# Kernel optimization log

Hardware: AMD Instinct MI355X
Metric: run time of the kernel (lower is better)

Reference implementation:

```python
import jax, jax.numpy as jnp
import numpy as np

B, N, K = 8, 4096, 16
C_IN = 3
MLP = (64, 64, 128)


def _init_conv(key, c_out, c_in):
    kw, kb = jax.random.split(key)
    bound = 1.0 / np.sqrt(c_in)
    W = jax.random.uniform(kw, (c_out, c_in), jnp.float32, -bound, bound)
    b = jax.random.uniform(kb, (c_out,), jnp.float32, -bound, bound)
    return W, b


def setup_inputs() -> dict:
    key = jax.random.key(0)
    k0, k1, k2, k3 = jax.random.split(key, 4)
    xyz = jax.random.normal(k0, (B, C_IN, N), jnp.float32)
    W0, b0 = _init_conv(k1, MLP[0], C_IN)
    W1, b1 = _init_conv(k2, MLP[1], MLP[0])
    W2, b2 = _init_conv(k3, MLP[2], MLP[1])
    return {"xyz": xyz, "W0": W0, "b0": b0, "W1": W1, "b1": b1, "W2": W2, "b2": b2}


def reference(xyz, W0, b0, W1, b1, W2, b2):
    # xyz: [B, 3, N] -> pts: [B, N, 3]
    pts = jnp.transpose(xyz, (0, 2, 1))
    # KNN: squared pairwise distances [B, N, N]
    sq = jnp.sum(pts * pts, axis=-1)  # [B, N]
    d2 = sq[:, :, None] + sq[:, None, :] - 2.0 * jnp.einsum('bnc,bmc->bnm', pts, pts)
    _, idx = jax.lax.top_k(-d2, K)  # [B, N, K] indices of K nearest (incl. self)
    # gather neighbor coords: [B, N, K, 3]
    grouped = jax.vmap(lambda p, i: p[i])(pts, idx)
    # center-relative coordinates
    rel = grouped - pts[:, :, None, :]  # [B, N, K, 3]
    # three 1x1 conv (= per-point linear) + ReLU layers
    h = jax.nn.relu(jnp.einsum('bnkc,oc->bnko', rel, W0) + b0)
    h = jax.nn.relu(jnp.einsum('bnkc,oc->bnko', h, W1) + b1)
    h = jax.nn.relu(jnp.einsum('bnkc,oc->bnko', h, W2) + b2)
    # max over K neighbors -> [B, N, D'] -> [B, D', N]
    out = jnp.max(h, axis=2)
    return jnp.transpose(out, (0, 2, 1))
```

## Files before the change

### kernel.cpp

```cpp
#include <hip/hip_runtime.h>
#include <cstddef>

#define NB   8
#define NPTS 4096
#define KNN  16
#define FCAP 64

typedef _Float16 h2 __attribute__((ext_vector_type(2)));
typedef _Float16 h8 __attribute__((ext_vector_type(8)));
typedef float    f4 __attribute__((ext_vector_type(4)));
typedef float    f16f __attribute__((ext_vector_type(16)));

static __device__ __forceinline__ h2 pk2(float a, float b) {
    return __builtin_bit_cast(h2, __builtin_amdgcn_cvt_pkrtz(a, b));
}
static __device__ __forceinline__ unsigned bch(h2 v) {
    return __builtin_bit_cast(unsigned, v);
}

#if __has_builtin(__builtin_amdgcn_fmed3f)
static __device__ __forceinline__ float MED3(float a, float b, float c) {
    return __builtin_amdgcn_fmed3f(a, b, c);
}
#else
static __device__ __forceinline__ float MED3(float a, float b, float c) {
    return fmaxf(fminf(a, b), fminf(fmaxf(a, b), c));
}
#endif

static __device__ __forceinline__ float dist2(float4 Q, float4 p) {
    float dot = fmaf(Q.z, p.z, fmaf(Q.y, p.y, Q.x * p.x));
    return fmaf(-2.0f, dot, Q.w + p.w);
}

__global__ __launch_bounds__(256) void prep_kernel(const float* __restrict__ xyz,
                                                   float4* __restrict__ pts4) {
    int i = blockIdx.x * 256 + threadIdx.x;
    int b = i >> 12;
    int n = i & (NPTS - 1);
    const float* base = xyz + (size_t)b * 3 * NPTS;
    float x = base[n];
    float y = base[NPTS + n];
    float z = base[2 * NPTS + n];
    float sq = fmaf(z, z, fmaf(y, y, x * x));
    pts4[i] = make_float4(x, y, z, sq);
}

__global__ __launch_bounds__(1024, 8) void knn_kernel(const float4* __restrict__ pts4,
                                                      int* __restrict__ idxout) {
    __shared__ uint2 Pm[NPTS];
    __shared__ char  sbuf[16384];
    __shared__ float tauv[64];
    __shared__ int   qcnt[64];
    __shared__ unsigned pmaxu, smaxu;

    float*    partials = (float*)sbuf;
    unsigned* fidx     = (unsigned*)sbuf;
    float*    fdist    = (float*)Pm;

    int tid = threadIdx.x;
    int b   = blockIdx.y;
    const float4* pb = pts4 + (size_t)b * NPTS;

    if (tid == 0) { pmaxu = 0u; smaxu = 0u; }
    __syncthreads();

    {
        float lm = 0.0f, ls = 0.0f;
        for (int j = tid; j < NPTS; j += 1024) {
            float4 p = pb[j];
            lm = fmaxf(lm, fmaxf(fabsf(p.x), fmaxf(fabsf(p.y), fabsf(p.z))));
            ls = fmaxf(ls, p.w);
            h2 lo = { (_Float16)p.x, (_Float16)p.y };
            h2 hi = { (_Float16)p.z, (_Float16)p.w };
            Pm[j].x = bch(lo);
            Pm[j].y = bch(hi);
        }
        atomicMax(&pmaxu, __builtin_bit_cast(unsigned, lm));
        atomicMax(&smaxu, __builtin_bit_cast(unsigned, ls));
    }

    int wave = tid >> 6, lane = tid & 63;
    int g  = wave >> 3;
    int c  = wave & 7;
    int col = lane & 31;
    int hl  = lane >> 5;
    int q  = g * 32 + col;
    int nq = (blockIdx.x << 6) + q;
    int cbase = c * 512;

    float4 qf = pb[nq];
    float uxf = -2.0f * qf.x, uyf = -2.0f * qf.y, uzf = -2.0f * qf.z;
    _Float16 uxh = (_Float16)uxf, uyh = (_Float16)uyf, uzh = (_Float16)uzf;
    _Float16 uxl = (_Float16)(uxf - (float)uxh);
    _Float16 uyl = (_Float16)(uyf - (float)uyh);
    _Float16 uzl = (_Float16)(uzf - (float)uzh);
    uint4 bu = {0u, 0u, 0u, 0u};
    if (hl == 0) {
        h2 b01 = {uxh, uyh}, b23 = {uzh, (_Float16)1.0f};
        h2 b45 = {uxl, uyl}, b67 = {uzl, (_Float16)0.0f};
        bu.x = bch(b01); bu.y = bch(b23); bu.z = bch(b45); bu.w = bch(b67);
    }
    h8 bq = __builtin_bit_cast(h8, bu);
    __syncthreads();

    {
        float c0 = __builtin_inff(), c1 = c0, c2 = c0, c3 = c0;
#pragma unroll 2
        for (int t = 0; t < 16; ++t) {
            uint4 au = {0u, 0u, 0u, 0u};
            if (hl == 0) {
                uint2 pd = Pm[cbase + t * 32 + col];
                au.x = pd.x; au.y = pd.y; au.z = pd.x; au.w = pd.y;
            }
            f16f d = __builtin_amdgcn_mfma_f32_32x32x16_f16(
                __builtin_bit_cast(h8, au), bq, (f16f)0.0f, 0, 0, 0);
            float a0 = fminf(d[0], d[1]),   a1 = fminf(d[2], d[3]);
            float a2 = fminf(d[4], d[5]),   a3 = fminf(d[6], d[7]);
            float a4 = fminf(d[8], d[9]),   a5 = fminf(d[10], d[11]);
            float a6 = fminf(d[12], d[13]), a7 = fminf(d[14], d[15]);
            float b0 = fminf(a0, a1), b1 = fminf(a2, a3);
            float b2 = fminf(a4, a5), b3 = fminf(a6, a7);
            float rmin = fminf(fminf(b0, b1), fminf(b2, b3));
            float p0 = c0, p1 = c1, p2 = c2;
            c0 = fminf(p0, rmin);
            c1 = MED3(rmin, p0, c1);
            c2 = MED3(rmin, p1, c2);
            c3 = MED3(rmin, p2, c3);
        }
        int sb = (c * 2 + hl) * 4;
        partials[(sb + 0) * 64 + q] = c0;
        partials[(sb + 1) * 64 + q] = c1;
        partials[(sb + 2) * 64 + q] = c2;
        partials[(sb + 3) * 64 + q] = c3;
    }
    __syncthreads();

    if (tid < 256) {
        int qq = tid & 63, k = tid >> 6;
        float mb[16];
#pragma unroll
        for (int j = 0; j < 16; ++j) mb[j] = __builtin_inff();
        for (int s = 0; s < 16; ++s) {
            float v = partials[(k * 16 + s) * 64 + qq];
            float prev = mb[0];
            mb[0] = fminf(mb[0], v);
#pragma unroll
            for (int i = 1; i < 16; ++i) {
                float cur = mb[i];
                mb[i] = MED3(v, prev, cur);
                prev = cur;
            }
        }
#pragma unroll
        for (int j = 0; j < 16; ++j) partials[(k * 16 + j) * 64 + qq] = mb[j];
    }
    __syncthreads();

    if (tid < 64) {
        float mb[16];
#pragma unroll
        for (int j = 0; j < 16; ++j) mb[j] = __builtin_inff();
        for (int k = 0; k < 4; ++k) {
            for (int j = 0; j < 16; ++j) {
                float v = partials[(k * 16 + j) * 64 + tid];
                if (v >= mb[15]) break;
                float prev = mb[0];
                mb[0] = fminf(mb[0], v);
#pragma unroll
                for (int i = 1; i < 16; ++i) {
                    float cur = mb[i];
                    mb[i] = MED3(v, prev, cur);
                    prev = cur;
                }
            }
        }
        float4 q2 = pb[(blockIdx.x << 6) + tid];
        float sumq = fabsf(q2.x) + fabsf(q2.y) + fabsf(q2.z);
        float qn   = sqrtf(q2.w);
        float pmax = __builtin_bit_cast(float, pmaxu);
        float smax = __builtin_bit_cast(float, smaxu);
        const float r11c = 4.8828125e-4f;
        float tau = mb[15];
        float E0  = smax * r11c + 2.0f * sumq * pmax * r11c + 1.0e-3f;
        float rad2 = fmaxf(tau + 2.0f * E0 + q2.w, 0.0f);
        float R   = qn + sqrtf(rad2);
        float Eq  = (R * R + 2.0f * sumq * R) * r11c + 6.0e-4f;
        Eq = fminf(Eq, E0);
        tauv[tid] = tau + 2.0f * Eq;
        qcnt[tid] = 0;
    }
    __syncthreads();

    {
        float tc = tauv[q];
#pragma unroll 1
        for (int t = 0; t < 16; ++t) {
            uint4 au = {0u, 0u, 0u, 0u};
            if (hl == 0) {
                uint2 pd = Pm[cbase + t * 32 + col];
                au.x = pd.x; au.y = pd.y; au.z = pd.x; au.w = pd.y;
            }
            f16f d = __builtin_amdgcn_mfma_f32_32x32x16_f16(
                __builtin_bit_cast(h8, au), bq, (f16f)0.0f, 0, 0, 0);
            unsigned m = 0u;
#pragma unroll
            for (int r = 0; r < 16; ++r) m |= (d[r] <= tc) ? (1u << r) : 0u;
            if (m) {
                int pos = atomicAdd(&qcnt[q], __popc(m));
                while (m) {
                    int r = __ffs(m) - 1;
                    m &= m - 1;
                    if (pos < FCAP)
                        fidx[pos * 64 + q] =
                            (unsigned)(cbase + t * 32 + (r & 3) + 8 * (r >> 2) + 4 * hl);
                    ++pos;
                }
            }
        }
    }
    __syncthreads();

    for (int e = tid; e < FCAP * 64; e += 1024) {
        int j = e >> 6, qq = e & 63;
        int nc = qcnt[qq]; nc = nc > FCAP ? FCAP : nc;
        if (j < nc) {
            float4 Qf = pb[(blockIdx.x << 6) + qq];
            fdist[e] = dist2(Qf, pb[fidx[e]]);
        }
    }
    __syncthreads();

    if (tid < 64) {
        int nqf = (blockIdx.x << 6) + tid;
        float4 Qf = pb[nqf];
        float bd[16]; int bi[16];
#pragma unroll
        for (int j = 0; j < 16; ++j) { bd[j] = __builtin_inff(); bi[j] = 0; }
        int cnt = qcnt[tid];
        if (cnt <= FCAP) {
            for (int j = 0; j < cnt; ++j) {
                float x  = fdist[j * 64 + tid];
                int   xi = (int)fidx[j * 64 + tid];
                if (x < bd[15] || (x == bd[15] && xi < bi[15])) {
#pragma unroll
                    for (int t = 0; t < 16; ++t) {
                        bool cc = (x < bd[t]) || (x == bd[t] && xi < bi[t]);
                        float nd = cc ? x  : bd[t];
                        int   ni = cc ? xi : bi[t];
                        float od = cc ? bd[t] : x;
                        int   oi = cc ? bi[t] : xi;
                        bd[t] = nd; bi[t] = ni; x = od; xi = oi;
                    }
                }
            }
        } else {
            for (int m = 0; m < NPTS; ++m) {
                float x = dist2(Qf, pb[m]);
                int  xi = m;
                if (x < bd[15] || (x == bd[15] && xi < bi[15])) {
#pragma unroll
                    for (int t = 0; t < 16; ++t) {
                        bool cc = (x < bd[t]) || (x == bd[t] && xi < bi[t]);
                        float nd = cc ? x  : bd[t];
                        int   ni = cc ? xi : bi[t];
                        float od = cc ? bd[t] : x;
                        int   oi = cc ? bi[t] : xi;
                        bd[t] = nd; bi[t] = ni; x = od; xi = oi;
                    }
                }
            }
        }
        int* op = idxout + ((size_t)b * NPTS + nqf) * KNN;
#pragma unroll
        for (int j = 0; j < 16; ++j) op[j] = bi[j];
    }
}

__global__ __launch_bounds__(256, 2) void mlp_kernel(
    const float4* __restrict__ pts4, const int* __restrict__ idxin,
    const float* __restrict__ W0, const float* __restrict__ b0,
    const float* __restrict__ W1, const float* __restrict__ b1,
    const float* __restrict__ W2, const float* __restrict__ b2,
    float* __restrict__ out) {

    int tid  = threadIdx.x;
    int wave = tid >> 6, lane = tid & 63;
    int g = lane >> 4, i = lane & 15;

    h2 w0x[8], w0y[8], w0z[8], w0b[8];
#pragma unroll
    for (int s = 0; s < 2; ++s)
#pragma unroll
        for (int v = 0; v < 4; ++v) {
            int c0 = 32 * s + 8 * g + 2 * v;
            w0x[s * 4 + v] = pk2(W0[c0 * 3 + 0], W0[c0 * 3 + 3]);
            w0y[s * 4 + v] = pk2(W0[c0 * 3 + 1], W0[c0 * 3 + 4]);
            w0z[s * 4 + v] = pk2(W0[c0 * 3 + 2], W0[c0 * 3 + 5]);
            w0b[s * 4 + v] = pk2(b0[c0], b0[c0 + 1]);
        }
    h2 b1p[8];
#pragma unroll
    for (int s = 0; s < 2; ++s)
#pragma unroll
        for (int v = 0; v < 4; ++v) {
            int c0 = 32 * s + 16 * (v >> 1) + 4 * g + 2 * (v & 1);
            b1p[s * 4 + v] = pk2(b1[c0], b1[c0 + 1]);
        }
    h8 wf1[4][2];
#pragma unroll
    for (int t = 0; t < 4; ++t)
#pragma unroll
        for (int s = 0; s < 2; ++s) {
            const float* p = W1 + (16 * t + i) * 64 + 32 * s + 8 * g;
            h8 f;
#pragma unroll
            for (int j = 0; j < 8; ++j) f[j] = (_Float16)p[j];
            wf1[t][s] = f;
        }
    h8 wf2[8][2];
#pragma unroll
    for (int t = 0; t < 8; ++t)
#pragma unroll
        for (int s = 0; s < 2; ++s) {
            const float* p = W2 + (16 * t + i) * 64;
            h8 f;
#pragma unroll
            for (int j = 0; j < 8; ++j) {
                int vc = 32 * s + 16 * (j >> 2) + 4 * g + (j & 3);
                f[j] = (_Float16)p[vc];
            }
            wf2[t][s] = f;
        }

    int gw = blockIdx.x * 4 + wave;
    int b  = gw >> 8;
    int n0 = (gw & 255) * 16;

    const float4* pb = pts4 + (size_t)b * NPTS;
    float4 q = pb[n0 + i];
    const int* ip = idxin + ((size_t)b * NPTS + n0 + i) * KNN;

    float mx[8][4];
#pragma unroll
    for (int t = 0; t < 8; ++t)
#pragma unroll
        for (int r = 0; r < 4; ++r) mx[t][r] = -3.4e38f;

    for (int it = 0; it < KNN; ++it) {
        int mi = ip[it];
        float4 p = pb[mi];
        float rx = p.x - q.x, ry = p.y - q.y, rz = p.z - q.z;
        h2 rxx = pk2(rx, rx), ryy = pk2(ry, ry), rzz = pk2(rz, rz);

        h8 h0f[2];
#pragma unroll
        for (int s = 0; s < 2; ++s)
#pragma unroll
            for (int v = 0; v < 4; ++v) {
                h2 hh = __builtin_elementwise_fma(w0z[s * 4 + v], rzz,
                         __builtin_elementwise_fma(w0y[s * 4 + v], ryy,
                          __builtin_elementwise_fma(w0x[s * 4 + v], rxx, w0b[s * 4 + v])));
                hh = __builtin_elementwise_max(hh, (h2)(_Float16)0.0f);
                h0f[s][2 * v]     = hh.x;
                h0f[s][2 * v + 1] = hh.y;
            }

        f4 d1[4];
#pragma unroll
        for (int t = 0; t < 4; ++t) {
            d1[t] = (f4)0.0f;
#pragma unroll
            for (int s = 0; s < 2; ++s)
                d1[t] = __builtin_amdgcn_mfma_f32_16x16x32_f16(wf1[t][s], h0f[s], d1[t], 0, 0, 0);
        }

        h8 h1f[2];
#pragma unroll
        for (int s = 0; s < 2; ++s)
#pragma unroll
            for (int v = 0; v < 4; ++v) {
                int t = 2 * s + (v >> 1), r0 = 2 * (v & 1);
                h2 w = pk2(d1[t][r0], d1[t][r0 + 1]);
                w = w + b1p[s * 4 + v];
                w = __builtin_elementwise_max(w, (h2)(_Float16)0.0f);
                h1f[s][2 * v]     = w.x;
                h1f[s][2 * v + 1] = w.y;
            }

#pragma unroll
        for (int t = 0; t < 8; ++t) {
            f4 d2 = (f4)0.0f;
#pragma unroll
            for (int s = 0; s < 2; ++s)
                d2 = __builtin_amdgcn_mfma_f32_16x16x32_f16(wf2[t][s], h1f[s], d2, 0, 0, 0);
#pragma unroll
            for (int r = 0; r < 4; ++r) mx[t][r] = fmaxf(mx[t][r], d2[r]);
        }
    }

    size_t ob = (size_t)b * 128 * NPTS + n0 + i;
#pragma unroll
    for (int t = 0; t < 8; ++t)
#pragma unroll
        for (int r = 0; r < 4; ++r) {
            int chn = 16 * t + 4 * g + r;
            float v = fmaxf(mx[t][r] + b2[chn], 0.0f);
            out[ob + (size_t)chn * NPTS] = v;
        }
}

extern "C" void kernel_launch(void* const* d_in, const int* in_sizes, int n_in,
                              void* d_out, int out_size, void* d_ws, size_t ws_size,
                              hipStream_t stream) {
    (void)in_sizes; (void)n_in; (void)out_size; (void)ws_size;
    const float* xyz = (const float*)d_in[0];
    const float* W0  = (const float*)d_in[1];
    const float* b0  = (const float*)d_in[2];
    const float* W1  = (const float*)d_in[3];
    const float* b1  = (const float*)d_in[4];
    const float* W2  = (const float*)d_in[5];
    const float* b2  = (const float*)d_in[6];
    float* out = (float*)d_out;

    char* ws = (char*)d_ws;
    float4* pts4 = (float4*)ws;
    int*    idxb = (int*)(ws + (size_t)NB * NPTS * sizeof(float4));

    prep_kernel<<<dim3(NB * NPTS / 256), dim3(256), 0, stream>>>(xyz, pts4);
    knn_kernel<<<dim3(NPTS / 64, NB), dim3(1024), 0, stream>>>(pts4, idxb);
    mlp_kernel<<<dim3(512), dim3(256), 0, stream>>>(
        pts4, idxb, W0, b0, W1, b1, W2, b2, out);
}
```

Measured before the change: 107.6 us.

## Precompute fp16 point table and bounds in prep, shrink KNN blocks to 32 queries

The prep kernel now runs one block per batch. It writes the packed fp16 point table and the per-batch max bounds to global memory, using a wave-shuffle reduction. The KNN kernel stops rebuilding the 32 KB shared fp16 table in every block and reads the MFMA operands straight from global/L2. Blocks shrink to 512 threads with 32 queries each, so there are twice as many blocks and far less shared memory per block. The costs are a prep kernel with only 8 blocks, which serialises more work, and global-memory latency on the MFMA operand loads.

```diff
diff --git a/kernel.cpp b/kernel.cpp
--- a/kernel.cpp
+++ b/kernel.cpp
@@ -5,6 +5,7 @@
 #define NPTS 4096
 #define KNN  16
 #define FCAP 64
+#define QB   32
 
 typedef _Float16 h2 __attribute__((ext_vector_type(2)));
 typedef _Float16 h8 __attribute__((ext_vector_type(8)));
@@ -33,60 +34,66 @@
     return fmaf(-2.0f, dot, Q.w + p.w);
 }
 
-__global__ __launch_bounds__(256) void prep_kernel(const float* __restrict__ xyz,
-                                                   float4* __restrict__ pts4) {
-    int i = blockIdx.x * 256 + threadIdx.x;
-    int b = i >> 12;
-    int n = i & (NPTS - 1);
+__global__ __launch_bounds__(1024) void prep_kernel(const float* __restrict__ xyz,
+                                                    float4* __restrict__ pts4,
+                                                    uint2* __restrict__ pm16,
+                                                    unsigned* __restrict__ mx) {
+    __shared__ float wred[32];
+    int b = blockIdx.x, tid = threadIdx.x;
     const float* base = xyz + (size_t)b * 3 * NPTS;
-    float x = base[n];
-    float y = base[NPTS + n];
-    float z = base[2 * NPTS + n];
-    float sq = fmaf(z, z, fmaf(y, y, x * x));
-    pts4[i] = make_float4(x, y, z, sq);
-}
-
-__global__ __launch_bounds__(1024, 8) void knn_kernel(const float4* __restrict__ pts4,
-                                                      int* __restrict__ idxout) {
-    __shared__ uint2 Pm[NPTS];
-    __shared__ char  sbuf[16384];
-    __shared__ float tauv[64];
-    __shared__ int   qcnt[64];
-    __shared__ unsigned pmaxu, smaxu;
+    float lm = 0.0f, ls = 0.0f;
+    for (int j = tid; j < NPTS; j += 1024) {
+        float x = base[j];
+        float y = base[NPTS + j];
+        float z = base[2 * NPTS + j];
+        float sq = fmaf(z, z, fmaf(y, y, x * x));
+        pts4[(size_t)b * NPTS + j] = make_float4(x, y, z, sq);
+        h2 lo = { (_Float16)x, (_Float16)y };
+        h2 hi = { (_Float16)z, (_Float16)sq };
+        pm16[(size_t)b * NPTS + j] = make_uint2(bch(lo), bch(hi));
+        lm = fmaxf(lm, fmaxf(fabsf(x), fmaxf(fabsf(y), fabsf(z))));
+        ls = fmaxf(ls, sq);
+    }
+#pragma unroll
+    for (int o = 32; o; o >>= 1) {
+        lm = fmaxf(lm, __shfl_xor(lm, o));
+        ls = fmaxf(ls, __shfl_xor(ls, o));
+    }
+    int wave = tid >> 6, lane = tid & 63;
+    if (lane == 0) { wred[wave] = lm; wred[16 + wave] = ls; }
+    __syncthreads();
+    if (tid == 0) {
+        float m = wred[0], s = wred[16];
+#pragma unroll
+        for (int i = 1; i < 16; ++i) { m = fmaxf(m, wred[i]); s = fmaxf(s, wred[16 + i]); }
+        mx[b * 2 + 0] = __builtin_bit_cast(unsigned, m);
+        mx[b * 2 + 1] = __builtin_bit_cast(unsigned, s);
+    }
+}
+
+__global__ __launch_bounds__(512, 8) void knn_kernel(const float4* __restrict__ pts4,
+                                                     const uint2* __restrict__ pm16,
+                                                     const unsigned* __restrict__ mx,
+                                                     int* __restrict__ idxout) {
+    __shared__ char  sbuf[8192];
+    __shared__ float fdist[FCAP * QB];
+    __shared__ float tauv[QB];
+    __shared__ int   qcnt[QB];
 
     float*    partials = (float*)sbuf;
     unsigned* fidx     = (unsigned*)sbuf;
-    float*    fdist    = (float*)Pm;
 
     int tid = threadIdx.x;
     int b   = blockIdx.y;
-    const float4* pb = pts4 + (size_t)b * NPTS;
-
-    if (tid == 0) { pmaxu = 0u; smaxu = 0u; }
-    __syncthreads();
-
-    {
-        float lm = 0.0f, ls = 0.0f;
-        for (int j = tid; j < NPTS; j += 1024) {
-            float4 p = pb[j];
-            lm = fmaxf(lm, fmaxf(fabsf(p.x), fmaxf(fabsf(p.y), fabsf(p.z))));
-            ls = fmaxf(ls, p.w);
-            h2 lo = { (_Float16)p.x, (_Float16)p.y };
-            h2 hi = { (_Float16)p.z, (_Float16)p.w };
-            Pm[j].x = bch(lo);
-            Pm[j].y = bch(hi);
-        }
-        atomicMax(&pmaxu, __builtin_bit_cast(unsigned, lm));
-        atomicMax(&smaxu, __builtin_bit_cast(unsigned, ls));
-    }
+    const float4* pb  = pts4 + (size_t)b * NPTS;
+    const uint2*  pmb = pm16 + (size_t)b * NPTS;
 
     int wave = tid >> 6, lane = tid & 63;
-    int g  = wave >> 3;
-    int c  = wave & 7;
+    int c   = wave;
     int col = lane & 31;
     int hl  = lane >> 5;
-    int q  = g * 32 + col;
-    int nq = (blockIdx.x << 6) + q;
+    int q   = col;
+    int nq  = blockIdx.x * QB + q;
     int cbase = c * 512;
 
     float4 qf = pb[nq];
@@ -102,7 +109,6 @@
         bu.x = bch(b01); bu.y = bch(b23); bu.z = bch(b45); bu.w = bch(b67);
     }
     h8 bq = __builtin_bit_cast(h8, bu);
-    __syncthreads();
 
     {
         float c0 = __builtin_inff(), c1 = c0, c2 = c0, c3 = c0;
@@ -110,7 +116,7 @@
         for (int t = 0; t < 16; ++t) {
             uint4 au = {0u, 0u, 0u, 0u};
             if (hl == 0) {
-                uint2 pd = Pm[cbase + t * 32 + col];
+                uint2 pd = pmb[cbase + t * 32 + col];
                 au.x = pd.x; au.y = pd.y; au.z = pd.x; au.w = pd.y;
             }
             f16f d = __builtin_amdgcn_mfma_f32_32x32x16_f16(
@@ -129,20 +135,20 @@
             c3 = MED3(rmin, p2, c3);
         }
         int sb = (c * 2 + hl) * 4;
-        partials[(sb + 0) * 64 + q] = c0;
-        partials[(sb + 1) * 64 + q] = c1;
-        partials[(sb + 2) * 64 + q] = c2;
-        partials[(sb + 3) * 64 + q] = c3;
-    }
-    __syncthreads();
-
-    if (tid < 256) {
-        int qq = tid & 63, k = tid >> 6;
+        partials[(sb + 0) * QB + q] = c0;
+        partials[(sb + 1) * QB + q] = c1;
+        partials[(sb + 2) * QB + q] = c2;
+        partials[(sb + 3) * QB + q] = c3;
+    }
+    __syncthreads();
+
+    if (tid < 4 * QB) {
+        int qq = tid & (QB - 1), k = tid >> 5;
         float mb[16];
 #pragma unroll
         for (int j = 0; j < 16; ++j) mb[j] = __builtin_inff();
         for (int s = 0; s < 16; ++s) {
-            float v = partials[(k * 16 + s) * 64 + qq];
+            float v = partials[(k * 16 + s) * QB + qq];
             float prev = mb[0];
             mb[0] = fminf(mb[0], v);
 #pragma unroll
@@ -153,17 +159,17 @@
             }
         }
 #pragma unroll
-        for (int j = 0; j < 16; ++j) partials[(k * 16 + j) * 64 + qq] = mb[j];
-    }
-    __syncthreads();
-
-    if (tid < 64) {
+        for (int j = 0; j < 16; ++j) partials[(k * 16 + j) * QB + qq] = mb[j];
+    }
+    __syncthreads();
+
+    if (tid < QB) {
         float mb[16];
 #pragma unroll
         for (int j = 0; j < 16; ++j) mb[j] = __builtin_inff();
         for (int k = 0; k < 4; ++k) {
             for (int j = 0; j < 16; ++j) {
-                float v = partials[(k * 16 + j) * 64 + tid];
+                float v = partials[(k * 16 + j) * QB + tid];
                 if (v >= mb[15]) break;
                 float prev = mb[0];
                 mb[0] = fminf(mb[0], v);
@@ -175,11 +181,11 @@
                 }
             }
         }
-        float4 q2 = pb[(blockIdx.x << 6) + tid];
+        float4 q2 = pb[blockIdx.x * QB + tid];
         float sumq = fabsf(q2.x) + fabsf(q2.y) + fabsf(q2.z);
         float qn   = sqrtf(q2.w);
-        float pmax = __builtin_bit_cast(float, pmaxu);
-        float smax = __builtin_bit_cast(float, smaxu);
+        float pmax = __builtin_bit_cast(float, mx[b * 2 + 0]);
+        float smax = __builtin_bit_cast(float, mx[b * 2 + 1]);
         const float r11c = 4.8828125e-4f;
         float tau = mb[15];
         float E0  = smax * r11c + 2.0f * sumq * pmax * r11c + 1.0e-3f;
@@ -198,7 +204,7 @@
         for (int t = 0; t < 16; ++t) {
             uint4 au = {0u, 0u, 0u, 0u};
             if (hl == 0) {
-                uint2 pd = Pm[cbase + t * 32 + col];
+                uint2 pd = pmb[cbase + t * 32 + col];
                 au.x = pd.x; au.y = pd.y; au.z = pd.x; au.w = pd.y;
             }
             f16f d = __builtin_amdgcn_mfma_f32_32x32x16_f16(
@@ -212,7 +218,7 @@
                     int r = __ffs(m) - 1;
                     m &= m - 1;
                     if (pos < FCAP)
-                        fidx[pos * 64 + q] =
+                        fidx[pos * QB + q] =
                             (unsigned)(cbase + t * 32 + (r & 3) + 8 * (r >> 2) + 4 * hl);
                     ++pos;
                 }
@@ -221,18 +227,18 @@
     }
     __syncthreads();
 
-    for (int e = tid; e < FCAP * 64; e += 1024) {
-        int j = e >> 6, qq = e & 63;
+    for (int e = tid; e < FCAP * QB; e += 512) {
+        int j = e >> 5, qq = e & (QB - 1);
         int nc = qcnt[qq]; nc = nc > FCAP ? FCAP : nc;
         if (j < nc) {
-            float4 Qf = pb[(blockIdx.x << 6) + qq];
+            float4 Qf = pb[blockIdx.x * QB + qq];
             fdist[e] = dist2(Qf, pb[fidx[e]]);
         }
     }
     __syncthreads();
 
-    if (tid < 64) {
-        int nqf = (blockIdx.x << 6) + tid;
+    if (tid < QB) {
+        int nqf = blockIdx.x * QB + tid;
         float4 Qf = pb[nqf];
         float bd[16]; int bi[16];
 #pragma unroll
@@ -240,8 +246,8 @@
         int cnt = qcnt[tid];
         if (cnt <= FCAP) {
             for (int j = 0; j < cnt; ++j) {
-                float x  = fdist[j * 64 + tid];
-                int   xi = (int)fidx[j * 64 + tid];
+                float x  = fdist[j * QB + tid];
+                int   xi = (int)fidx[j * QB + tid];
                 if (x < bd[15] || (x == bd[15] && xi < bi[15])) {
 #pragma unroll
                     for (int t = 0; t < 16; ++t) {
@@ -424,11 +430,13 @@
     float* out = (float*)d_out;
 
     char* ws = (char*)d_ws;
-    float4* pts4 = (float4*)ws;
-    int*    idxb = (int*)(ws + (size_t)NB * NPTS * sizeof(float4));
-
-    prep_kernel<<<dim3(NB * NPTS / 256), dim3(256), 0, stream>>>(xyz, pts4);
-    knn_kernel<<<dim3(NPTS / 64, NB), dim3(1024), 0, stream>>>(pts4, idxb);
+    float4*   pts4 = (float4*)ws;
+    int*      idxb = (int*)(ws + (512 << 10));
+    uint2*    pm16 = (uint2*)(ws + (512 << 10) + (2 << 20));
+    unsigned* mxb  = (unsigned*)(ws + (512 << 10) + (2 << 20) + (256 << 10));
+
+    prep_kernel<<<dim3(NB), dim3(1024), 0, stream>>>(xyz, pts4, pm16, mxb);
+    knn_kernel<<<dim3(NPTS / QB, NB), dim3(512), 0, stream>>>(pts4, pm16, mxb, idxb);
     mlp_kernel<<<dim3(512), dim3(256), 0, stream>>>(
         pts4, idxb, W0, b0, W1, b1, W2, b2, out);
 }
```

Result: faster. 97.12 us (-9.7%).
